# Kernel optimization log

Measured on AMD Instinct MI355X. Metric: run time of the kernel, lower is better.

The kernel has to match this reference:

```python
import jax, jax.numpy as jnp
import numpy as np

# Hyper-parameters (defaults of EnergyHyperParameters)
BETA = 1.0
ALPHA = 1.0
LAMBDA_L2 = 0.01
LAMBDA_SMOOTH = 0.001  # unused: compute_grad defaults to False so grad_z is None


def setup_inputs() -> dict:
    key = jax.random.key(0)
    k1, k2, k3 = jax.random.split(key, 3)
    B, N, D = 4096, 65536, 256
    z = jax.random.normal(k1, (B, D), dtype=jnp.float32)
    z_next = jax.random.normal(k2, (B, D), dtype=jnp.float32)
    memory_patterns = jax.random.normal(k3, (N, D), dtype=jnp.float32)
    return {"z": z, "z_next": z_next, "memory_patterns": memory_patterns}


def reference(z, z_next, memory_patterns):
    # Hopfield energy: -logsumexp(beta * z @ M^T) per row, then mean
    logits = BETA * jnp.einsum("bd,nd->bn", z, memory_patterns)  # [B, N]
    hopfield = jnp.mean(-jax.nn.logsumexp(logits, axis=-1))
    # DEQ consistency: alpha * mean ||z - z_next||^2
    consistency = ALPHA * jnp.mean(jnp.sum((z - z_next) ** 2, axis=-1))
    # Regularization: lambda_l2 * mean ||z||^2 (no smoothness term, grad_z is None)
    regularization = LAMBDA_L2 * jnp.mean(jnp.sum(z * z, axis=-1))
    total = hopfield + consistency + regularization
    return (total, hopfield, consistency, regularization)
```

## Files before the change

kernel.cpp:

```cpp
#include <hip/hip_runtime.h>
#include <stdint.h>


typedef __attribute__((ext_vector_type(8))) int   v8i;
typedef __attribute__((ext_vector_type(4))) float f32x4;

#define N_PAT  65536
#define D_DIM  256
#define B_ROWS 4096
#define NSPLIT 16
#define NRANGE (N_PAT / NSPLIT)
#define SPR    (NRANGE / 16)
#define SPERW  (SPR / 2)
#define BBLK   128
#define SHIFT2 69.0f
#define LOG2E  1.44269504f
#define LN2    0.69314718f
#define SCL1   0x7F7F7F7F

#define WS_M_OFF   ((size_t)0)
#define WS_M_BYTES ((size_t)N_PAT * D_DIM)
#define WS_Z_OFF   (WS_M_OFF + WS_M_BYTES)
#define WS_Z_BYTES ((size_t)B_ROWS * D_DIM)
#define WS_LSE_OFF (WS_Z_OFF + WS_Z_BYTES)
#define WS_LSE_BYTES ((size_t)B_ROWS * NSPLIT * 2 * 4)
#define WS_CSS_OFF (WS_LSE_OFF + WS_LSE_BYTES)
#define WS_ZSS_OFF (WS_CSS_OFF + (size_t)512 * 4)

__device__ __forceinline__ float fexp2(float x) {
  return __builtin_amdgcn_exp2f(x);
}

__device__ __forceinline__ int pk4_fp8(float a, float b, float c, float d) {
  int r = __builtin_amdgcn_cvt_pk_fp8_f32(a, b, 0, false);
  r = __builtin_amdgcn_cvt_pk_fp8_f32(c, d, r, true);
  return r;
}

__device__ __forceinline__ float waveRedAdd(float v) {
  #pragma unroll
  for (int o = 32; o > 0; o >>= 1) v += __shfl_down(v, o, 64);
  return v;
}

__global__ void convert_m_kernel(const float* __restrict__ src, int* __restrict__ dst) {
  const int c = blockIdx.x * 256 + threadIdx.x;
  const int row = c >> 5;
  const int j = c & 31;
  const float* sp = src + (size_t)row * D_DIM + j * 8;
  const float4 x = *(const float4*)(sp);
  const float4 y = *(const float4*)(sp + 4);
  int2 o;
  o.x = pk4_fp8(x.x, x.y, x.z, x.w);
  o.y = pk4_fp8(y.x, y.y, y.z, y.w);
  const size_t dw = (size_t)(row >> 4) * 1024 + (j >> 4) * 512 +
                    (((j >> 2) & 3) * 16 + (row & 15)) * 8 + (j & 3) * 2;
  *(int2*)(dst + dw) = o;
}

__global__ void prep_z_kernel(const float* __restrict__ z, const float* __restrict__ zn,
                              int* __restrict__ z8, float* __restrict__ css,
                              float* __restrict__ zss) {
  int t = blockIdx.x * 256 + threadIdx.x;
  const float* az = z + (size_t)t * 8;
  const float* an = zn + (size_t)t * 8;
  float4 z0 = *(const float4*)(az), z1 = *(const float4*)(az + 4);
  float4 n0 = *(const float4*)(an), n1 = *(const float4*)(an + 4);
  float zv[8] = {z0.x, z0.y, z0.z, z0.w, z1.x, z1.y, z1.z, z1.w};
  float nv[8] = {n0.x, n0.y, n0.z, n0.w, n1.x, n1.y, n1.z, n1.w};
  float cs = 0.f, zs = 0.f;
  #pragma unroll
  for (int j = 0; j < 8; ++j) {
    float d = zv[j] - nv[j];
    cs += d * d;
    zs += zv[j] * zv[j];
  }
  int2 o;
  o.x = pk4_fp8(zv[0] * LOG2E, zv[1] * LOG2E, zv[2] * LOG2E, zv[3] * LOG2E);
  o.y = pk4_fp8(zv[4] * LOG2E, zv[5] * LOG2E, zv[6] * LOG2E, zv[7] * LOG2E);
  *(int2*)(z8 + (size_t)t * 2) = o;

  __shared__ float rc[4], rz[4];
  cs = waveRedAdd(cs);
  zs = waveRedAdd(zs);
  int w = threadIdx.x >> 6, lane = threadIdx.x & 63;
  if (lane == 0) { rc[w] = cs; rz[w] = zs; }
  __syncthreads();
  if (threadIdx.x == 0) {
    css[blockIdx.x] = rc[0] + rc[1] + rc[2] + rc[3];
    zss[blockIdx.x] = rz[0] + rz[1] + rz[2] + rz[3];
  }
}

__global__ __launch_bounds__(256, 2) void lse_kernel(const int* __restrict__ Mp,
                                                     const int* __restrict__ z8,
                                                     float* __restrict__ lsep) {
  const int bid = blockIdx.x;
  const int xcd = bid & 7;
  const int g = bid >> 3;
  const int bblk = g & 31;
  const int half = g >> 5;
  const int nsplit = xcd * 2 + half;

  const int tid = threadIdx.x;
  const int w = tid >> 6;
  const int lane = tid & 63;
  const int l15 = lane & 15;
  const int grp = lane >> 4;
  const int bh = w & 1;
  const int nh = w >> 1;

  if (half) __builtin_amdgcn_s_sleep(5);

  v8i zf[4][2];
  const int brow0 = bblk * BBLK + bh * 64;
  #pragma unroll
  for (int bt = 0; bt < 4; ++bt) {
    #pragma unroll
    for (int kh = 0; kh < 2; ++kh) {
      int row = brow0 + bt * 16 + l15;
      zf[bt][kh] = *(const v8i*)(z8 + (size_t)row * 64 + kh * 32 + grp * 8);
    }
  }

  const int* pj = Mp + (size_t)(nsplit * SPR + nh) * 1024 + lane * 8;

  float ssum[4] = {0.f, 0.f, 0.f, 0.f};
  f32x4 accA[4], accB[4];
  v8i afA[2], afB[2];

  #pragma unroll
  for (int bt = 0; bt < 4; ++bt)
    #pragma unroll
    for (int q = 0; q < 4; ++q) accB[bt][q] = -INFINITY;

  #pragma unroll
  for (int kh = 0; kh < 2; ++kh) afA[kh] = *(const v8i*)(pj + kh * 512);

  auto body = [&](f32x4 (&CUR)[4], f32x4 (&PREV)[4], v8i (&CURF)[2], v8i (&NXTF)[2]) {
    const int* pn = pj + 2048;
    #pragma unroll
    for (int kh = 0; kh < 2; ++kh) NXTF[kh] = *(const v8i*)(pn + kh * 512);

    #pragma unroll
    for (int bt = 0; bt < 4; ++bt)
      #pragma unroll
      for (int q = 0; q < 4; ++q) CUR[bt][q] = -SHIFT2;

    __builtin_amdgcn_s_setprio(1);
    #pragma unroll
    for (int kh = 0; kh < 2; ++kh)
      #pragma unroll
      for (int bt = 0; bt < 4; ++bt)
        CUR[bt] = __builtin_amdgcn_mfma_scale_f32_16x16x128_f8f6f4(
            CURF[kh], zf[bt][kh], CUR[bt], 0, 0, 0, SCL1, 0, SCL1);
    __builtin_amdgcn_s_setprio(0);

    #pragma unroll
    for (int bt = 0; bt < 4; ++bt)
      ssum[bt] += (fexp2(PREV[bt][0]) + fexp2(PREV[bt][1])) +
                  (fexp2(PREV[bt][2]) + fexp2(PREV[bt][3]));

    pj = pn;
  };

  #pragma unroll 1
  for (int jp = 0; jp < SPERW / 2; ++jp) {
    body(accA, accB, afA, afB);
    body(accB, accA, afB, afA);
  }

  #pragma unroll
  for (int bt = 0; bt < 4; ++bt)
    ssum[bt] += (fexp2(accB[bt][0]) + fexp2(accB[bt][1])) +
                (fexp2(accB[bt][2]) + fexp2(accB[bt][3]));

  #pragma unroll
  for (int bt = 0; bt < 4; ++bt) {
    ssum[bt] += __shfl_xor(ssum[bt], 16, 64);
    ssum[bt] += __shfl_xor(ssum[bt], 32, 64);
  }
  if (grp == 0) {
    #pragma unroll
    for (int bt = 0; bt < 4; ++bt) {
      int b = brow0 + bt * 16 + l15;
      lsep[(size_t)b * (NSPLIT * 2) + nsplit * 2 + nh] = ssum[bt];
    }
  }
}

__global__ void finalize_kernel(const float* __restrict__ lsep, const float* __restrict__ css,
                                const float* __restrict__ zss, float* __restrict__ out) {
  __shared__ float r1[16], r2[16], r3[16];
  int tid = threadIdx.x;
  float sum_lse = 0.f;
  for (int r = tid; r < B_ROWS; r += 1024) {
    float S = 0.f;
    #pragma unroll
    for (int i = 0; i < NSPLIT * 2; ++i) S += lsep[(size_t)r * (NSPLIT * 2) + i];
    sum_lse += SHIFT2 * LN2 + logf(S);
  }
  float cs = 0.f, zs = 0.f;
  if (tid < 512) { cs = css[tid]; zs = zss[tid]; }

  sum_lse = waveRedAdd(sum_lse);
  cs = waveRedAdd(cs);
  zs = waveRedAdd(zs);
  int w = tid >> 6, lane = tid & 63;
  if (lane == 0) { r1[w] = sum_lse; r2[w] = cs; r3[w] = zs; }
  __syncthreads();
  if (tid == 0) {
    float sl = 0.f, sc = 0.f, sz = 0.f;
    #pragma unroll
    for (int i = 0; i < 16; ++i) { sl += r1[i]; sc += r2[i]; sz += r3[i]; }
    float hop = -sl / (float)B_ROWS;
    float cons = sc / (float)B_ROWS;
    float reg = 0.01f * sz / (float)B_ROWS;
    out[0] = hop + cons + reg;
    out[1] = hop;
    out[2] = cons;
    out[3] = reg;
  }
}

extern "C" void kernel_launch(void* const* d_in, const int* in_sizes, int n_in,
                              void* d_out, int out_size, void* d_ws, size_t ws_size,
                              hipStream_t stream) {
  (void)in_sizes; (void)n_in; (void)out_size; (void)ws_size;
  const float* z  = (const float*)d_in[0];
  const float* zn = (const float*)d_in[1];
  const float* M  = (const float*)d_in[2];
  char* ws = (char*)d_ws;
  int* Mp  = (int*)(ws + WS_M_OFF);
  int* z8  = (int*)(ws + WS_Z_OFF);
  float* lsep = (float*)(ws + WS_LSE_OFF);
  float* css = (float*)(ws + WS_CSS_OFF);
  float* zss = (float*)(ws + WS_ZSS_OFF);

  convert_m_kernel<<<8192, 256, 0, stream>>>(M, Mp);
  prep_z_kernel<<<512, 256, 0, stream>>>(z, zn, z8, css, zss);
  lse_kernel<<<512, 256, 0, stream>>>(Mp, z8, lsep);
  finalize_kernel<<<1, 1024, 0, stream>>>(lsep, css, zss, (float*)d_out);
}
```

Baseline: 95.45 us.

## Split row logsumexp into parallel kernel, drop sleep, seed MFMA with constant

The per-row sum over the 32 partial sums and its log move out of the single-block finalize kernel into a new 16-block kernel, which writes one value per row. Finalize then only sums these row values. The staggered s_sleep for the second-half blocks is removed, and the first MFMA of each tile takes a constant -SHIFT2 accumulator instead of a per-iteration register initialisation. The change trades one extra kernel launch for more parallel tail work and a slightly leaner inner loop.

```diff
diff --git a/kernel.cpp b/kernel.cpp
--- a/kernel.cpp
+++ b/kernel.cpp
@@ -13,6 +13,7 @@
 #define SPR    (NRANGE / 16)
 #define SPERW  (SPR / 2)
 #define BBLK   128
+#define NPART  (NSPLIT * 2)
 #define SHIFT2 69.0f
 #define LOG2E  1.44269504f
 #define LN2    0.69314718f
@@ -23,8 +24,10 @@
 #define WS_Z_OFF   (WS_M_OFF + WS_M_BYTES)
 #define WS_Z_BYTES ((size_t)B_ROWS * D_DIM)
 #define WS_LSE_OFF (WS_Z_OFF + WS_Z_BYTES)
-#define WS_LSE_BYTES ((size_t)B_ROWS * NSPLIT * 2 * 4)
-#define WS_CSS_OFF (WS_LSE_OFF + WS_LSE_BYTES)
+#define WS_LSE_BYTES ((size_t)B_ROWS * NPART * 4)
+#define WS_ROW_OFF (WS_LSE_OFF + WS_LSE_BYTES)
+#define WS_ROW_BYTES ((size_t)B_ROWS * 4)
+#define WS_CSS_OFF (WS_ROW_OFF + WS_ROW_BYTES)
 #define WS_ZSS_OFF (WS_CSS_OFF + (size_t)512 * 4)
 
 __device__ __forceinline__ float fexp2(float x) {
@@ -110,8 +113,6 @@
   const int bh = w & 1;
   const int nh = w >> 1;
 
-  if (half) __builtin_amdgcn_s_sleep(5);
-
   v8i zf[4][2];
   const int brow0 = bblk * BBLK + bh * 64;
   #pragma unroll
@@ -125,6 +126,7 @@
 
   const int* pj = Mp + (size_t)(nsplit * SPR + nh) * 1024 + lane * 8;
 
+  const f32x4 INITC = {-SHIFT2, -SHIFT2, -SHIFT2, -SHIFT2};
   float ssum[4] = {0.f, 0.f, 0.f, 0.f};
   f32x4 accA[4], accB[4];
   v8i afA[2], afB[2];
@@ -142,18 +144,15 @@
     #pragma unroll
     for (int kh = 0; kh < 2; ++kh) NXTF[kh] = *(const v8i*)(pn + kh * 512);
 
+    __builtin_amdgcn_s_setprio(1);
     #pragma unroll
     for (int bt = 0; bt < 4; ++bt)
-      #pragma unroll
-      for (int q = 0; q < 4; ++q) CUR[bt][q] = -SHIFT2;
-
-    __builtin_amdgcn_s_setprio(1);
-    #pragma unroll
-    for (int kh = 0; kh < 2; ++kh)
-      #pragma unroll
-      for (int bt = 0; bt < 4; ++bt)
-        CUR[bt] = __builtin_amdgcn_mfma_scale_f32_16x16x128_f8f6f4(
-            CURF[kh], zf[bt][kh], CUR[bt], 0, 0, 0, SCL1, 0, SCL1);
+      CUR[bt] = __builtin_amdgcn_mfma_scale_f32_16x16x128_f8f6f4(
+          CURF[0], zf[bt][0], INITC, 0, 0, 0, SCL1, 0, SCL1);
+    #pragma unroll
+    for (int bt = 0; bt < 4; ++bt)
+      CUR[bt] = __builtin_amdgcn_mfma_scale_f32_16x16x128_f8f6f4(
+          CURF[1], zf[bt][1], CUR[bt], 0, 0, 0, SCL1, 0, SCL1);
     __builtin_amdgcn_s_setprio(0);
 
     #pragma unroll
@@ -184,22 +183,26 @@
     #pragma unroll
     for (int bt = 0; bt < 4; ++bt) {
       int b = brow0 + bt * 16 + l15;
-      lsep[(size_t)b * (NSPLIT * 2) + nsplit * 2 + nh] = ssum[bt];
+      lsep[(size_t)b * NPART + nsplit * 2 + nh] = ssum[bt];
     }
   }
 }
 
-__global__ void finalize_kernel(const float* __restrict__ lsep, const float* __restrict__ css,
+__global__ void rowlse_kernel(const float* __restrict__ lsep, float* __restrict__ rowlse) {
+  int r = blockIdx.x * 256 + threadIdx.x;
+  float S = 0.f;
+  #pragma unroll
+  for (int i = 0; i < NPART; ++i) S += lsep[(size_t)r * NPART + i];
+  rowlse[r] = SHIFT2 * LN2 + logf(S);
+}
+
+__global__ void finalize_kernel(const float* __restrict__ rowlse, const float* __restrict__ css,
                                 const float* __restrict__ zss, float* __restrict__ out) {
   __shared__ float r1[16], r2[16], r3[16];
   int tid = threadIdx.x;
   float sum_lse = 0.f;
-  for (int r = tid; r < B_ROWS; r += 1024) {
-    float S = 0.f;
-    #pragma unroll
-    for (int i = 0; i < NSPLIT * 2; ++i) S += lsep[(size_t)r * (NSPLIT * 2) + i];
-    sum_lse += SHIFT2 * LN2 + logf(S);
-  }
+  #pragma unroll
+  for (int i = 0; i < 4; ++i) sum_lse += rowlse[tid + i * 1024];
   float cs = 0.f, zs = 0.f;
   if (tid < 512) { cs = css[tid]; zs = zss[tid]; }
 
@@ -234,11 +237,13 @@
   int* Mp  = (int*)(ws + WS_M_OFF);
   int* z8  = (int*)(ws + WS_Z_OFF);
   float* lsep = (float*)(ws + WS_LSE_OFF);
+  float* rowlse = (float*)(ws + WS_ROW_OFF);
   float* css = (float*)(ws + WS_CSS_OFF);
   float* zss = (float*)(ws + WS_ZSS_OFF);
 
   convert_m_kernel<<<8192, 256, 0, stream>>>(M, Mp);
   prep_z_kernel<<<512, 256, 0, stream>>>(z, zn, z8, css, zss);
   lse_kernel<<<512, 256, 0, stream>>>(Mp, z8, lsep);
-  finalize_kernel<<<1, 1024, 0, stream>>>(lsep, css, zss, (float*)d_out);
-}
+  rowlse_kernel<<<16, 256, 0, stream>>>(lsep, rowlse);
+  finalize_kernel<<<1, 1024, 0, stream>>>(rowlse, css, zss, (float*)d_out);
+}
```

Result: faster. 83.88 us (-12.1%).
